# Performance work log

Hardware: AMD Instinct MI355X
Metric: run time of the kernel (lower is better)

Reference implementation:

```python
import jax, jax.numpy as jnp
import numpy as np

SELF_OBS_DIM = 18
NBR_OBS_DIM = 6
K = 6          # num_use_neighbor_obs
H = 128        # neighbor_hidden_size
B = 65536


def _mlp2(x, w1, b1, w2, b2):
    # two fc layers each followed by tanh nonlinearity
    x = jnp.tanh(x @ w1 + b1)
    return jnp.tanh(x @ w2 + b2)


def setup_inputs() -> dict:
    key = jax.random.key(0)
    ks = jax.random.split(key, 12)

    def w(k, i, o):
        return jax.random.normal(k, (i, o), dtype=jnp.float32) * (1.0 / np.sqrt(i))

    return {
        "self_obs": jax.random.normal(ks[0], (B, SELF_OBS_DIM), dtype=jnp.float32),
        "obs": jax.random.normal(ks[1], (B, SELF_OBS_DIM + K * NBR_OBS_DIM), dtype=jnp.float32),
        # embedding_mlp: (self_obs_dim + nbr_obs_dim) -> H -> H
        "e_w1": w(ks[2], SELF_OBS_DIM + NBR_OBS_DIM, H), "e_b1": jnp.zeros((H,), jnp.float32),
        "e_w2": w(ks[3], H, H), "e_b2": jnp.zeros((H,), jnp.float32),
        # neighbor_value_mlp: H -> H -> H
        "v_w1": w(ks[4], H, H), "v_b1": jnp.zeros((H,), jnp.float32),
        "v_w2": w(ks[5], H, H), "v_b2": jnp.zeros((H,), jnp.float32),
        # attention_mlp: 2H -> H -> H -> 1
        "a_w1": w(ks[6], 2 * H, H), "a_b1": jnp.zeros((H,), jnp.float32),
        "a_w2": w(ks[7], H, H), "a_b2": jnp.zeros((H,), jnp.float32),
        "a_w3": w(ks[8], H, 1), "a_b3": jnp.zeros((1,), jnp.float32),
        "all_neighbor_obs_size": K * NBR_OBS_DIM,
        "batch_size": B,
    }


def reference(self_obs, obs, e_w1, e_b1, e_w2, e_b2, v_w1, v_b1, v_w2, v_b2,
              a_w1, a_b1, a_w2, a_b2, a_w3, a_b3, all_neighbor_obs_size, batch_size):
    # slice neighbor obs and flatten: row i -> (batch i//K, neighbor i%K)
    obs_neighbors = obs[:, SELF_OBS_DIM:SELF_OBS_DIM + all_neighbor_obs_size]
    obs_neighbors = obs_neighbors.reshape(-1, NBR_OBS_DIM)            # [B*K, 6]
    # torch .repeat(K, 1): tile whole batch K times -> row i -> batch i % B
    self_obs_repeat = jnp.tile(self_obs, (K, 1))                       # [B*K, 18]
    mlp_input = jnp.concatenate((self_obs_repeat, obs_neighbors), axis=1)

    neighbor_embeddings = _mlp2(mlp_input, e_w1, e_b1, e_w2, e_b2)     # [B*K, H]
    neighbor_values = _mlp2(neighbor_embeddings, v_w1, v_b1, v_w2, v_b2)

    emb_mean = jnp.mean(neighbor_embeddings.reshape(batch_size, -1, H), axis=1)  # [B, H]
    emb_mean_repeat = jnp.tile(emb_mean, (K, 1))                       # [B*K, H]

    att_in = jnp.concatenate((neighbor_embeddings, emb_mean_repeat), axis=1)     # [B*K, 2H]
    att_h = jnp.tanh(att_in @ a_w1 + a_b1)
    att_h = jnp.tanh(att_h @ a_w2 + a_b2)
    att_logits = (att_h @ a_w3 + a_b3).reshape(batch_size, -1)         # [B, K]

    att = jax.nn.softmax(att_logits, axis=1).reshape(-1, 1)            # [B*K, 1]
    weighted = (att * neighbor_values).reshape(batch_size, -1, H)      # [B, K, H]
    return jnp.sum(weighted, axis=1)                                   # [B, H]
```

## Files before the change

### kernel.cpp

```cpp
#include <hip/hip_runtime.h>

typedef _Float16 f16;
typedef f16   f16x8 __attribute__((ext_vector_type(8)));
typedef float f32x4 __attribute__((ext_vector_type(4)));
typedef unsigned int uint;

#define NB     65536
#define TPB    16

#define OFF_E1 0
#define OFF_E2 4096
#define OFF_V1 20480
#define OFF_V2 36864
#define OFF_A1 53248
#define OFF_A2 86016
#define WFRAG_TOTAL 102400

#define EMB_BYTE_OFF   204800ull
#define PERM_BYTE_OFF  (204800ull + 100663296ull)

#define LDS_FENCE() asm volatile("s_waitcnt lgkmcnt(0)" ::: "memory")
#define WAIT_VM0()  asm volatile("s_waitcnt vmcnt(0)" ::: "memory")
#define BAR()       { __builtin_amdgcn_s_barrier(); __builtin_amdgcn_sched_barrier(0); }
#define SBAR()      __builtin_amdgcn_sched_barrier(0)

__device__ __forceinline__ float tanh_fast(float x) {
  float e = __expf(2.0f * x);
  return 1.0f - 2.0f * __builtin_amdgcn_rcpf(e + 1.0f);
}

__global__ void prep_weights(const float* __restrict__ e1, const float* __restrict__ e2,
                             const float* __restrict__ v1, const float* __restrict__ v2,
                             const float* __restrict__ a1, const float* __restrict__ a2,
                             f16* __restrict__ dst)
{
  int i = blockIdx.x * 256 + threadIdx.x;
  if (i >= WFRAG_TOTAL) return;
  const float* src; int base, Ksrc;
  if      (i < OFF_E2) { src = e1; base = OFF_E1; Ksrc = 24;  }
  else if (i < OFF_V1) { src = e2; base = OFF_E2; Ksrc = 128; }
  else if (i < OFF_V2) { src = v1; base = OFF_V1; Ksrc = 128; }
  else if (i < OFF_A1) { src = v2; base = OFF_V2; Ksrc = 128; }
  else if (i < OFF_A2) { src = a1; base = OFF_A1; Ksrc = 256; }
  else                 { src = a2; base = OFF_A2; Ksrc = 128; }
  int li   = i - base;
  int j    = li & 7;
  int lane = (li >> 3) & 63;
  int nt   = (li >> 9) & 7;
  int kc   = li >> 12;
  int k = kc*32 + (lane >> 4)*8 + j;
  int n = nt*16 + (lane & 15);
  float v = (k < Ksrc) ? src[k*128 + n] : 0.0f;
  dst[i] = (f16)v;
}

__device__ __forceinline__ void mfma2(f32x4* acc, f16x8 a0, f16x8 a1, const f16* Wb, int lane)
{
  #pragma unroll
  for (int nt = 0; nt < 8; ++nt) {
    f16x8 w = *(const f16x8*)(Wb + (nt*64 + lane)*8);
    acc[nt] = __builtin_amdgcn_mfma_f32_16x16x32_f16(a0, w, acc[nt], 0, 0, 0);
  }
  #pragma unroll
  for (int nt = 0; nt < 8; ++nt) {
    f16x8 w = *(const f16x8*)(Wb + ((8+nt)*64 + lane)*8);
    acc[nt] = __builtin_amdgcn_mfma_f32_16x16x32_f16(a1, w, acc[nt], 0, 0, 0);
  }
}

__device__ __forceinline__ void epi_tanh_store(char* tb, const f32x4* acc, const float* bias8,
                                               int wid, int lane)
{
  int col0 = lane & 15, q = lane >> 4;
  #pragma unroll
  for (int nt = 0; nt < 8; ++nt) {
    #pragma unroll
    for (int rg = 0; rg < 4; ++rg) {
      int row = wid*16 + q*4 + rg;
      float h = tanh_fast(acc[nt][rg] + bias8[nt]);
      int byte = (row*256 + (nt*16 + col0)*2) ^ ((row & 7) << 4);
      *(f16*)(tb + byte) = (f16)h;
    }
  }
}

__device__ __forceinline__ void read_h_frags(const char* tb, f16x8* frag, int wid, int lane)
{
  int c = lane >> 4, rr = lane & 15;
  int row = wid*16 + rr;
  #pragma unroll
  for (int kc = 0; kc < 4; ++kc) {
    int byte = (row*256 + kc*64 + c*16) ^ ((row & 7) << 4);
    frag[kc] = *(const f16x8*)(tb + byte);
  }
}

__device__ __forceinline__ void gload_lds16(const f16* g, f16* l) {
  __builtin_amdgcn_global_load_lds(
    (const __attribute__((address_space(1))) unsigned int*)g,
    (__attribute__((address_space(3))) unsigned int*)l, 16, 0, 0);
}
__device__ __forceinline__ void stage32(const f16* g, f16* l, int tid) {
  #pragma unroll
  for (int it = 0; it < 6; ++it) {
    int idx = (tid + it*384) & 2047;
    gload_lds16(g + idx*8, l + idx*8);
  }
}
__device__ __forceinline__ void stageE1(const f16* g, f16* l, int tid) {
  #pragma unroll
  for (int it = 0; it < 2; ++it) {
    int idx = (tid + it*384) & 511;
    gload_lds16(g + idx*8, l + idx*8);
  }
}

__device__ __forceinline__ f16x8 gather_x(const float* __restrict__ so, const float* __restrict__ obs,
                                          int r, int c)
{
  int rs = r & (NB - 1);
  uint rq = (uint)r / 6u;
  uint rm = (uint)r - rq*6u;
  float xv[8] = {0.f,0.f,0.f,0.f,0.f,0.f,0.f,0.f};
  if (c == 0) {
    #pragma unroll
    for (int j = 0; j < 8; ++j) xv[j] = so[rs*18 + j];
  } else if (c == 1) {
    #pragma unroll
    for (int j = 0; j < 8; ++j) xv[j] = so[rs*18 + 8 + j];
  } else if (c == 2) {
    xv[0] = so[rs*18 + 16];
    xv[1] = so[rs*18 + 17];
    const float* nb = obs + (size_t)rq*54 + 18 + rm*6;
    #pragma unroll
    for (int j = 0; j < 6; ++j) xv[2+j] = nb[j];
  }
  f16x8 f;
  #pragma unroll
  for (int j = 0; j < 8; ++j) f[j] = (f16)xv[j];
  return f;
}

__global__ void __launch_bounds__(384, 1) enc_kernel(
  const float* __restrict__ self_obs, const float* __restrict__ obs,
  const float* __restrict__ e_b1, const float* __restrict__ e_b2,
  const float* __restrict__ a_b1,
  const f16* __restrict__ wfrag, f16* __restrict__ emb_out, f16* __restrict__ perm_out)
{
  __shared__ __align__(16) f16 E1b[4096];
  __shared__ __align__(16) f16 E2b[16384];
  __shared__ __align__(16) f16 A1m[16384];
  __shared__ __align__(16) char tbuf[24576];
  __shared__ __align__(16) char mbuf[24576];

  int tid = threadIdx.x, lane = tid & 63, wid = tid >> 6;
  int c = lane >> 4, rr = lane & 15;

  stageE1(wfrag + OFF_E1, E1b, tid);
  stage32(wfrag + OFF_E2, E2b, tid);
  stage32(wfrag + OFF_A1 + 16384, A1m, tid);

  float eb1r[8], eb2r[8], ab1r[8];
  #pragma unroll
  for (int nt = 0; nt < 8; ++nt) {
    int col = nt*16 + rr;
    eb1r[nt] = e_b1[col]; eb2r[nt] = e_b2[col]; ab1r[nt] = a_b1[col];
  }

  int S = blockIdx.x;
  int T0 = S*6;
  int jmax = 4096 - T0; if (jmax > 6) jmax = 6;

  f16x8 xfrag = gather_x(self_obs, obs, T0*96 + wid*16 + rr, c);
  WAIT_VM0(); BAR();

  for (int j = 0; j < jmax; ++j) {
    int T = T0 + j;
    f32x4 acc1[8];
    #pragma unroll
    for (int nt = 0; nt < 8; ++nt) acc1[nt] = (f32x4){0.f,0.f,0.f,0.f};
    #pragma unroll
    for (int nt = 0; nt < 8; ++nt) {
      f16x8 w = *(const f16x8*)(E1b + (nt*64 + lane)*8);
      acc1[nt] = __builtin_amdgcn_mfma_f32_16x16x32_f16(xfrag, w, acc1[nt], 0, 0, 0);
    }
    epi_tanh_store(tbuf, acc1, eb1r, wid, lane);
    LDS_FENCE();
    f16x8 hf[4];
    read_h_frags(tbuf, hf, wid, lane);

    f16x8 xnext = xfrag;
    if (j + 1 < jmax) xnext = gather_x(self_obs, obs, (T+1)*96 + wid*16 + rr, c);

    f32x4 acc2[8];
    #pragma unroll
    for (int nt = 0; nt < 8; ++nt) acc2[nt] = (f32x4){0.f,0.f,0.f,0.f};
    mfma2(acc2, hf[0], hf[1], E2b,        lane);
    mfma2(acc2, hf[2], hf[3], E2b + 8192, lane);
    epi_tanh_store(tbuf, acc2, eb2r, wid, lane);
    LDS_FENCE();

    {
      size_t gbase = (size_t)T * (96*128);
      #pragma unroll
      for (int it = 0; it < 4; ++it) {
        int idx = it*64 + lane;
        int row = wid*16 + (idx >> 4), ch = idx & 15;
        int byte = (row*256 + ch*16) ^ ((row & 7) << 4);
        *(uint4*)(emb_out + gbase + (size_t)row*128 + ch*8) = *(const uint4*)(tbuf + byte);
      }
    }
    BAR();
    for (int i2 = tid; i2 < 1024; i2 += 384) {
      int b = i2 >> 6, cp = i2 & 63;
      float s0 = 0.f, s1 = 0.f;
      #pragma unroll
      for (int k2 = 0; k2 < 6; ++k2) {
        int brow = b*6 + k2;
        uint v = *(const uint*)(tbuf + ((brow*256 + cp*4) ^ ((brow & 7) << 4)));
        s0 += (float)__builtin_bit_cast(f16, (unsigned short)(v & 0xffff));
        s1 += (float)__builtin_bit_cast(f16, (unsigned short)(v >> 16));
      }
      f16 h0 = (f16)(s0 * (1.0f/6.0f)), h1 = (f16)(s1 * (1.0f/6.0f));
      uint mv = (uint)__builtin_bit_cast(unsigned short, h0)
              | ((uint)__builtin_bit_cast(unsigned short, h1) << 16);
      int mrow = j*16 + b;
      *(uint*)(mbuf + ((mrow*256 + cp*4) ^ ((mrow & 7) << 4))) = mv;
    }
    LDS_FENCE(); BAR();
    xfrag = xnext;
  }

  f16x8 mfr[4];
  read_h_frags(mbuf, mfr, wid, lane);
  f32x4 accm[8];
  #pragma unroll
  for (int nt = 0; nt < 8; ++nt) accm[nt] = (f32x4){0.f,0.f,0.f,0.f};
  mfma2(accm, mfr[0], mfr[1], A1m,        lane);
  mfma2(accm, mfr[2], mfr[3], A1m + 8192, lane);

  int gbase = S*96;
  #pragma unroll
  for (int rg = 0; rg < 4; ++rg) {
    int m = gbase + wid*16 + c*4 + rg;
    if (m < NB) {
      f16x8 v;
      #pragma unroll
      for (int nt = 0; nt < 8; ++nt) v[nt] = (f16)(accm[nt][rg] + ab1r[nt]);
      *(f16x8*)(perm_out + (size_t)m*128 + rr*8) = v;
    }
  }
}

__global__ void __launch_bounds__(384, 1) att_kernel(
  const f16* __restrict__ wfrag, const f16* __restrict__ emb, const f16* __restrict__ perm,
  const float* __restrict__ a_b2, const float* __restrict__ a_w3, const float* __restrict__ a_b3,
  const float* __restrict__ v_b1, const float* __restrict__ v_b2,
  float* __restrict__ out)
{
  __shared__ __align__(16) f16 W[4][16384];
  __shared__ __align__(16) char tbuf[24576];
  __shared__ float attv[96];

  int tid = threadIdx.x, lane = tid & 63, wid = tid >> 6;
  int c = lane >> 4, rr = lane & 15;

  stage32(wfrag + OFF_A1, &W[0][0], tid);
  stage32(wfrag + OFF_A2, &W[1][0], tid);
  stage32(wfrag + OFF_V1, &W[2][0], tid);
  stage32(wfrag + OFF_V2, &W[3][0], tid);

  float ab2r[8], aw3r[8], vb1r[8], vb2r[8];
  #pragma unroll
  for (int nt = 0; nt < 8; ++nt) {
    int col = nt*16 + rr;
    ab2r[nt] = a_b2[col]; aw3r[nt] = a_w3[col]; vb1r[nt] = v_b1[col]; vb2r[nt] = v_b2[col];
  }
  float ab3r = a_b3[0];

  int t0 = blockIdx.x * TPB;
  f16x8 ef[4], mh[4];
  {
    size_t r = (size_t)t0*96 + wid*16 + rr;
    #pragma unroll
    for (int kc = 0; kc < 4; ++kc) ef[kc] = *(const f16x8*)(emb + r*128 + kc*32 + c*8);
    #pragma unroll
    for (int rg = 0; rg < 4; ++rg) {
      int m = (t0*96 + wid*16 + c*4 + rg) & (NB - 1);
      mh[rg] = *(const f16x8*)(perm + (size_t)m*128 + rr*8);
    }
  }
  WAIT_VM0(); BAR();

  for (int i = 0; i < TPB; ++i) {
    int t = t0 + i;

    f32x4 acc3[8];
    #pragma unroll
    for (int nt = 0; nt < 8; ++nt) acc3[nt] = (f32x4){0.f,0.f,0.f,0.f};
    mfma2(acc3, ef[0], ef[1], &W[0][0],    lane);
    mfma2(acc3, ef[2], ef[3], &W[0][8192], lane);

    f16x8 efn[4], mhn[4];
    {
      int tn = (i+1 < TPB) ? (t+1) : t;
      size_t r = (size_t)tn*96 + wid*16 + rr;
      #pragma unroll
      for (int kc = 0; kc < 4; ++kc) efn[kc] = *(const f16x8*)(emb + r*128 + kc*32 + c*8);
      #pragma unroll
      for (int rg = 0; rg < 4; ++rg) {
        int m = (tn*96 + wid*16 + c*4 + rg) & (NB - 1);
        mhn[rg] = *(const f16x8*)(perm + (size_t)m*128 + rr*8);
      }
    }

    #pragma unroll
    for (int nt = 0; nt < 8; ++nt) {
      #pragma unroll
      for (int rg = 0; rg < 4; ++rg) {
        int row = wid*16 + c*4 + rg;
        float h = tanh_fast(acc3[nt][rg] + (float)mh[rg][nt]);
        int byte = (row*256 + (nt*16 + rr)*2) ^ ((row & 7) << 4);
        *(f16*)(tbuf + byte) = (f16)h;
      }
    }
    LDS_FENCE();
    f16x8 hf[4];
    read_h_frags(tbuf, hf, wid, lane);

    f32x4 acc4[8];
    #pragma unroll
    for (int nt = 0; nt < 8; ++nt) acc4[nt] = (f32x4){0.f,0.f,0.f,0.f};
    mfma2(acc4, hf[0], hf[1], &W[1][0],    lane);
    mfma2(acc4, hf[2], hf[3], &W[1][8192], lane);

    float part[4] = {0.f,0.f,0.f,0.f};
    #pragma unroll
    for (int nt = 0; nt < 8; ++nt) {
      #pragma unroll
      for (int rg = 0; rg < 4; ++rg) part[rg] += tanh_fast(acc4[nt][rg] + ab2r[nt]) * aw3r[nt];
    }
    #pragma unroll
    for (int rg = 0; rg < 4; ++rg) {
      part[rg] += __shfl_xor(part[rg], 1);
      part[rg] += __shfl_xor(part[rg], 2);
      part[rg] += __shfl_xor(part[rg], 4);
      part[rg] += __shfl_xor(part[rg], 8);
    }
    if (rr == 0) {
      #pragma unroll
      for (int rg = 0; rg < 4; ++rg) attv[wid*16 + c*4 + rg] = part[rg] + ab3r;
    }
    LDS_FENCE(); BAR();
    if (tid < 16) {
      float l[6]; float m = -1e30f;
      #pragma unroll
      for (int k2 = 0; k2 < 6; ++k2) { l[k2] = attv[tid*6 + k2]; m = fmaxf(m, l[k2]); }
      float ss = 0.f;
      #pragma unroll
      for (int k2 = 0; k2 < 6; ++k2) { l[k2] = __expf(l[k2] - m); ss += l[k2]; }
      float inv = __builtin_amdgcn_rcpf(ss);
      #pragma unroll
      for (int k2 = 0; k2 < 6; ++k2) attv[tid*6 + k2] = l[k2] * inv;
    }
    LDS_FENCE(); BAR();
    float attw[4];
    #pragma unroll
    for (int rg = 0; rg < 4; ++rg) attw[rg] = attv[wid*16 + c*4 + rg];

    f32x4 acc5[8];
    #pragma unroll
    for (int nt = 0; nt < 8; ++nt) acc5[nt] = (f32x4){0.f,0.f,0.f,0.f};
    mfma2(acc5, ef[0], ef[1], &W[2][0],    lane);
    mfma2(acc5, ef[2], ef[3], &W[2][8192], lane);
    epi_tanh_store(tbuf, acc5, vb1r, wid, lane);
    LDS_FENCE();
    read_h_frags(tbuf, hf, wid, lane);

    f32x4 acc6[8];
    #pragma unroll
    for (int nt = 0; nt < 8; ++nt) acc6[nt] = (f32x4){0.f,0.f,0.f,0.f};
    mfma2(acc6, hf[0], hf[1], &W[3][0],    lane);
    mfma2(acc6, hf[2], hf[3], &W[3][8192], lane);

    #pragma unroll
    for (int nt = 0; nt < 8; ++nt) {
      #pragma unroll
      for (int rg = 0; rg < 4; ++rg) {
        int brow = wid*16 + c*4 + rg;
        float v = tanh_fast(acc6[nt][rg] + vb2r[nt]) * attw[rg];
        int byte = (brow*256 + (nt*16 + rr)*2) ^ ((brow & 7) << 4);
        *(f16*)(tbuf + byte) = (f16)v;
      }
    }
    LDS_FENCE(); BAR();

    int b0 = t*16;
    for (int i2 = tid; i2 < 1024; i2 += 384) {
      int b = i2 >> 6, cp = i2 & 63;
      float s0 = 0.f, s1 = 0.f;
      #pragma unroll
      for (int k2 = 0; k2 < 6; ++k2) {
        int brow = b*6 + k2;
        uint v = *(const uint*)(tbuf + ((brow*256 + cp*4) ^ ((brow & 7) << 4)));
        s0 += (float)__builtin_bit_cast(f16, (unsigned short)(v & 0xffff));
        s1 += (float)__builtin_bit_cast(f16, (unsigned short)(v >> 16));
      }
      float2 st = {s0, s1};
      *(float2*)(out + (size_t)(b0 + b)*128 + cp*2) = st;
    }
    BAR();

    #pragma unroll
    for (int kc = 0; kc < 4; ++kc) ef[kc] = efn[kc];
    #pragma unroll
    for (int rg = 0; rg < 4; ++rg) mh[rg] = mhn[rg];
  }
}

extern "C" void kernel_launch(void* const* d_in, const int* in_sizes, int n_in,
                              void* d_out, int out_size, void* d_ws, size_t ws_size,
                              hipStream_t stream)
{
  const float* self_obs = (const float*)d_in[0];
  const float* obs  = (const float*)d_in[1];
  const float* e_w1 = (const float*)d_in[2];
  const float* e_b1 = (const float*)d_in[3];
  const float* e_w2 = (const float*)d_in[4];
  const float* e_b2 = (const float*)d_in[5];
  const float* v_w1 = (const float*)d_in[6];
  const float* v_b1 = (const float*)d_in[7];
  const float* v_w2 = (const float*)d_in[8];
  const float* v_b2 = (const float*)d_in[9];
  const float* a_w1 = (const float*)d_in[10];
  const float* a_b1 = (const float*)d_in[11];
  const float* a_w2 = (const float*)d_in[12];
  const float* a_b2 = (const float*)d_in[13];
  const float* a_w3 = (const float*)d_in[14];
  const float* a_b3 = (const float*)d_in[15];

  f16*   wfrag = (f16*)d_ws;
  f16*   emb   = (f16*)((char*)d_ws + EMB_BYTE_OFF);
  f16*   perm  = (f16*)((char*)d_ws + PERM_BYTE_OFF);
  float* out   = (float*)d_out;

  prep_weights<<<400, 256, 0, stream>>>(e_w1, e_w2, v_w1, v_w2, a_w1, a_w2, wfrag);
  enc_kernel<<<683, 384, 0, stream>>>(self_obs, obs, e_b1, e_b2, a_b1, wfrag, emb, perm);
  att_kernel<<<256, 384, 0, stream>>>(wfrag, emb, perm, a_b2, a_w3, a_b3, v_b1, v_b2, out);
}
```

Baseline: 332.1 us.

## Make attention kernel wave-independent with per-wave jobs and in-register softmax

Restructures the attention kernel so each wave owns a 48-row job (8 batch items) with its own LDS scratch buffer. Softmax runs in registers through shuffles, and output sums are accumulated per wave, which removes the block-wide barriers and the shared attv buffer. It moves to 7 waves per block and drops the a_b3 bias, since softmax is shift invariant. It also drops the next-tile register prefetch of emb/perm, so global load latency is exposed inside each job, and raises register pressure with three chunks of fragments held live.

```diff
diff --git a/kernel.cpp b/kernel.cpp
--- a/kernel.cpp
+++ b/kernel.cpp
@@ -22,7 +22,6 @@
 #define LDS_FENCE() asm volatile("s_waitcnt lgkmcnt(0)" ::: "memory")
 #define WAIT_VM0()  asm volatile("s_waitcnt vmcnt(0)" ::: "memory")
 #define BAR()       { __builtin_amdgcn_s_barrier(); __builtin_amdgcn_sched_barrier(0); }
-#define SBAR()      __builtin_amdgcn_sched_barrier(0)
 
 __device__ __forceinline__ float tanh_fast(float x) {
   float e = __expf(2.0f * x);
@@ -252,23 +251,34 @@
   }
 }
 
-__global__ void __launch_bounds__(384, 1) att_kernel(
+#define NWAVE  7
+#define AITERS 5
+#define NJOBS  8192
+
+__global__ void __launch_bounds__(448, 1) att_kernel(
   const f16* __restrict__ wfrag, const f16* __restrict__ emb, const f16* __restrict__ perm,
-  const float* __restrict__ a_b2, const float* __restrict__ a_w3, const float* __restrict__ a_b3,
+  const float* __restrict__ a_b2, const float* __restrict__ a_w3,
   const float* __restrict__ v_b1, const float* __restrict__ v_b2,
   float* __restrict__ out)
 {
   __shared__ __align__(16) f16 W[4][16384];
-  __shared__ __align__(16) char tbuf[24576];
-  __shared__ float attv[96];
+  __shared__ __align__(16) char tbuf[NWAVE][4096];
 
   int tid = threadIdx.x, lane = tid & 63, wid = tid >> 6;
   int c = lane >> 4, rr = lane & 15;
 
-  stage32(wfrag + OFF_A1, &W[0][0], tid);
-  stage32(wfrag + OFF_A2, &W[1][0], tid);
-  stage32(wfrag + OFF_V1, &W[2][0], tid);
-  stage32(wfrag + OFF_V2, &W[3][0], tid);
+  {
+    const int offs[4] = {OFF_A1, OFF_A2, OFF_V1, OFF_V2};
+    #pragma unroll
+    for (int m = 0; m < 4; ++m) {
+      const f16* s = wfrag + offs[m];
+      #pragma unroll
+      for (int it = 0; it < 5; ++it) {
+        int idx = (tid + it*448) & 2047;
+        gload_lds16(s + idx*8, &W[m][0] + idx*8);
+      }
+    }
+  }
 
   float ab2r[8], aw3r[8], vb1r[8], vb2r[8];
   #pragma unroll
@@ -276,145 +286,163 @@
     int col = nt*16 + rr;
     ab2r[nt] = a_b2[col]; aw3r[nt] = a_w3[col]; vb1r[nt] = v_b1[col]; vb2r[nt] = v_b2[col];
   }
-  float ab3r = a_b3[0];
-
-  int t0 = blockIdx.x * TPB;
-  f16x8 ef[4], mh[4];
-  {
-    size_t r = (size_t)t0*96 + wid*16 + rr;
-    #pragma unroll
-    for (int kc = 0; kc < 4; ++kc) ef[kc] = *(const f16x8*)(emb + r*128 + kc*32 + c*8);
-    #pragma unroll
-    for (int rg = 0; rg < 4; ++rg) {
-      int m = (t0*96 + wid*16 + c*4 + rg) & (NB - 1);
-      mh[rg] = *(const f16x8*)(perm + (size_t)m*128 + rr*8);
-    }
-  }
+
   WAIT_VM0(); BAR();
 
-  for (int i = 0; i < TPB; ++i) {
-    int t = t0 + i;
-
-    f32x4 acc3[8];
-    #pragma unroll
-    for (int nt = 0; nt < 8; ++nt) acc3[nt] = (f32x4){0.f,0.f,0.f,0.f};
-    mfma2(acc3, ef[0], ef[1], &W[0][0],    lane);
-    mfma2(acc3, ef[2], ef[3], &W[0][8192], lane);
-
-    f16x8 efn[4], mhn[4];
-    {
-      int tn = (i+1 < TPB) ? (t+1) : t;
-      size_t r = (size_t)tn*96 + wid*16 + rr;
-      #pragma unroll
-      for (int kc = 0; kc < 4; ++kc) efn[kc] = *(const f16x8*)(emb + r*128 + kc*32 + c*8);
+  char* tb = (char*)&tbuf[wid][0];
+
+  for (int it = 0; it < AITERS; ++it) {
+    int job = (blockIdx.x * AITERS + it) * NWAVE + wid;
+    if (job >= NJOBS) break;
+    int rbase = job * 48;
+
+    f16x8 ef[3][4];
+    float E[3][4];
+    #pragma unroll
+    for (int ch = 0; ch < 3; ++ch) {
+      int ra = rbase + ch*16 + rr;
+      #pragma unroll
+      for (int kc = 0; kc < 4; ++kc)
+        ef[ch][kc] = *(const f16x8*)(emb + (size_t)ra*128 + kc*32 + c*8);
+      f16x8 mh[4];
       #pragma unroll
       for (int rg = 0; rg < 4; ++rg) {
-        int m = (tn*96 + wid*16 + c*4 + rg) & (NB - 1);
-        mhn[rg] = *(const f16x8*)(perm + (size_t)m*128 + rr*8);
-      }
-    }
-
-    #pragma unroll
-    for (int nt = 0; nt < 8; ++nt) {
+        int m = (rbase + ch*16 + c*4 + rg) & (NB - 1);
+        mh[rg] = *(const f16x8*)(perm + (size_t)m*128 + rr*8);
+      }
+      f32x4 acc[8];
+      #pragma unroll
+      for (int nt = 0; nt < 8; ++nt) acc[nt] = (f32x4){0.f,0.f,0.f,0.f};
+      mfma2(acc, ef[ch][0], ef[ch][1], &W[0][0],    lane);
+      mfma2(acc, ef[ch][2], ef[ch][3], &W[0][8192], lane);
+      #pragma unroll
+      for (int nt = 0; nt < 8; ++nt) {
+        #pragma unroll
+        for (int rg = 0; rg < 4; ++rg) {
+          int row = c*4 + rg;
+          float h = tanh_fast(acc[nt][rg] + (float)mh[rg][nt]);
+          *(f16*)(tb + ((row*256 + (nt*16 + rr)*2) ^ ((row & 7) << 4))) = (f16)h;
+        }
+      }
+      LDS_FENCE();
+      f16x8 hf[4];
+      #pragma unroll
+      for (int kc = 0; kc < 4; ++kc)
+        hf[kc] = *(const f16x8*)(tb + ((rr*256 + kc*64 + c*16) ^ ((rr & 7) << 4)));
+      f32x4 acc2[8];
+      #pragma unroll
+      for (int nt = 0; nt < 8; ++nt) acc2[nt] = (f32x4){0.f,0.f,0.f,0.f};
+      mfma2(acc2, hf[0], hf[1], &W[1][0],    lane);
+      mfma2(acc2, hf[2], hf[3], &W[1][8192], lane);
+      float part[4] = {0.f,0.f,0.f,0.f};
+      #pragma unroll
+      for (int nt = 0; nt < 8; ++nt) {
+        #pragma unroll
+        for (int rg = 0; rg < 4; ++rg)
+          part[rg] += tanh_fast(acc2[nt][rg] + ab2r[nt]) * aw3r[nt];
+      }
       #pragma unroll
       for (int rg = 0; rg < 4; ++rg) {
-        int row = wid*16 + c*4 + rg;
-        float h = tanh_fast(acc3[nt][rg] + (float)mh[rg][nt]);
-        int byte = (row*256 + (nt*16 + rr)*2) ^ ((row & 7) << 4);
-        *(f16*)(tbuf + byte) = (f16)h;
-      }
-    }
-    LDS_FENCE();
-    f16x8 hf[4];
-    read_h_frags(tbuf, hf, wid, lane);
-
-    f32x4 acc4[8];
-    #pragma unroll
-    for (int nt = 0; nt < 8; ++nt) acc4[nt] = (f32x4){0.f,0.f,0.f,0.f};
-    mfma2(acc4, hf[0], hf[1], &W[1][0],    lane);
-    mfma2(acc4, hf[2], hf[3], &W[1][8192], lane);
-
-    float part[4] = {0.f,0.f,0.f,0.f};
-    #pragma unroll
-    for (int nt = 0; nt < 8; ++nt) {
-      #pragma unroll
-      for (int rg = 0; rg < 4; ++rg) part[rg] += tanh_fast(acc4[nt][rg] + ab2r[nt]) * aw3r[nt];
-    }
-    #pragma unroll
-    for (int rg = 0; rg < 4; ++rg) {
-      part[rg] += __shfl_xor(part[rg], 1);
-      part[rg] += __shfl_xor(part[rg], 2);
-      part[rg] += __shfl_xor(part[rg], 4);
-      part[rg] += __shfl_xor(part[rg], 8);
-    }
-    if (rr == 0) {
-      #pragma unroll
-      for (int rg = 0; rg < 4; ++rg) attv[wid*16 + c*4 + rg] = part[rg] + ab3r;
-    }
-    LDS_FENCE(); BAR();
-    if (tid < 16) {
-      float l[6]; float m = -1e30f;
-      #pragma unroll
-      for (int k2 = 0; k2 < 6; ++k2) { l[k2] = attv[tid*6 + k2]; m = fmaxf(m, l[k2]); }
-      float ss = 0.f;
-      #pragma unroll
-      for (int k2 = 0; k2 < 6; ++k2) { l[k2] = __expf(l[k2] - m); ss += l[k2]; }
-      float inv = __builtin_amdgcn_rcpf(ss);
-      #pragma unroll
-      for (int k2 = 0; k2 < 6; ++k2) attv[tid*6 + k2] = l[k2] * inv;
-    }
-    LDS_FENCE(); BAR();
-    float attw[4];
-    #pragma unroll
-    for (int rg = 0; rg < 4; ++rg) attw[rg] = attv[wid*16 + c*4 + rg];
-
-    f32x4 acc5[8];
-    #pragma unroll
-    for (int nt = 0; nt < 8; ++nt) acc5[nt] = (f32x4){0.f,0.f,0.f,0.f};
-    mfma2(acc5, ef[0], ef[1], &W[2][0],    lane);
-    mfma2(acc5, ef[2], ef[3], &W[2][8192], lane);
-    epi_tanh_store(tbuf, acc5, vb1r, wid, lane);
-    LDS_FENCE();
-    read_h_frags(tbuf, hf, wid, lane);
-
-    f32x4 acc6[8];
-    #pragma unroll
-    for (int nt = 0; nt < 8; ++nt) acc6[nt] = (f32x4){0.f,0.f,0.f,0.f};
-    mfma2(acc6, hf[0], hf[1], &W[3][0],    lane);
-    mfma2(acc6, hf[2], hf[3], &W[3][8192], lane);
-
-    #pragma unroll
-    for (int nt = 0; nt < 8; ++nt) {
+        part[rg] += __shfl_xor(part[rg], 1);
+        part[rg] += __shfl_xor(part[rg], 2);
+        part[rg] += __shfl_xor(part[rg], 4);
+        part[rg] += __shfl_xor(part[rg], 8);
+        E[ch][rg] = __expf(part[rg]);
+      }
+    }
+
+    int g = rr & 7;
+    float pg = 0.f;
+    #pragma unroll
+    for (int ch = 0; ch < 3; ++ch) {
       #pragma unroll
       for (int rg = 0; rg < 4; ++rg) {
-        int brow = wid*16 + c*4 + rg;
-        float v = tanh_fast(acc6[nt][rg] + vb2r[nt]) * attw[rg];
-        int byte = (brow*256 + (nt*16 + rr)*2) ^ ((brow & 7) << 4);
-        *(f16*)(tbuf + byte) = (f16)v;
-      }
-    }
-    LDS_FENCE(); BAR();
-
-    int b0 = t*16;
-    for (int i2 = tid; i2 < 1024; i2 += 384) {
-      int b = i2 >> 6, cp = i2 & 63;
-      float s0 = 0.f, s1 = 0.f;
-      #pragma unroll
-      for (int k2 = 0; k2 < 6; ++k2) {
-        int brow = b*6 + k2;
-        uint v = *(const uint*)(tbuf + ((brow*256 + cp*4) ^ ((brow & 7) << 4)));
-        s0 += (float)__builtin_bit_cast(f16, (unsigned short)(v & 0xffff));
-        s1 += (float)__builtin_bit_cast(f16, (unsigned short)(v >> 16));
-      }
-      float2 st = {s0, s1};
-      *(float2*)(out + (size_t)(b0 + b)*128 + cp*2) = st;
-    }
-    BAR();
-
-    #pragma unroll
-    for (int kc = 0; kc < 4; ++kc) ef[kc] = efn[kc];
-    #pragma unroll
-    for (int rg = 0; rg < 4; ++rg) mh[rg] = mhn[rg];
+        int r = ch*16 + c*4 + rg;
+        pg += (r/6 == g) ? E[ch][rg] : 0.f;
+      }
+    }
+    pg += __shfl_xor(pg, 16);
+    pg += __shfl_xor(pg, 32);
+    float invS = __builtin_amdgcn_rcpf(pg);
+    float attw[3][4];
+    #pragma unroll
+    for (int ch = 0; ch < 3; ++ch) {
+      #pragma unroll
+      for (int rg = 0; rg < 4; ++rg) {
+        int r = ch*16 + c*4 + rg;
+        attw[ch][rg] = E[ch][rg] * __shfl(invS, r/6);
+      }
+    }
+
+    float o0x=0.f,o0y=0.f,o1x=0.f,o1y=0.f,o2x=0.f,o2y=0.f,o3x=0.f,o3y=0.f;
+    float o4x=0.f,o4y=0.f,o5x=0.f,o5y=0.f,o6x=0.f,o6y=0.f,o7x=0.f,o7y=0.f;
+    #pragma unroll
+    for (int ch = 0; ch < 3; ++ch) {
+      f32x4 acc3[8];
+      #pragma unroll
+      for (int nt = 0; nt < 8; ++nt) acc3[nt] = (f32x4){0.f,0.f,0.f,0.f};
+      mfma2(acc3, ef[ch][0], ef[ch][1], &W[2][0],    lane);
+      mfma2(acc3, ef[ch][2], ef[ch][3], &W[2][8192], lane);
+      #pragma unroll
+      for (int nt = 0; nt < 8; ++nt) {
+        #pragma unroll
+        for (int rg = 0; rg < 4; ++rg) {
+          int row = c*4 + rg;
+          float h = tanh_fast(acc3[nt][rg] + vb1r[nt]);
+          *(f16*)(tb + ((row*256 + (nt*16 + rr)*2) ^ ((row & 7) << 4))) = (f16)h;
+        }
+      }
+      LDS_FENCE();
+      f16x8 hf[4];
+      #pragma unroll
+      for (int kc = 0; kc < 4; ++kc)
+        hf[kc] = *(const f16x8*)(tb + ((rr*256 + kc*64 + c*16) ^ ((rr & 7) << 4)));
+      f32x4 acc4[8];
+      #pragma unroll
+      for (int nt = 0; nt < 8; ++nt) acc4[nt] = (f32x4){0.f,0.f,0.f,0.f};
+      mfma2(acc4, hf[0], hf[1], &W[3][0],    lane);
+      mfma2(acc4, hf[2], hf[3], &W[3][8192], lane);
+      #pragma unroll
+      for (int nt = 0; nt < 8; ++nt) {
+        #pragma unroll
+        for (int rg = 0; rg < 4; ++rg) {
+          int row = c*4 + rg;
+          float v = tanh_fast(acc4[nt][rg] + vb2r[nt]) * attw[ch][rg];
+          *(f16*)(tb + ((row*256 + (nt*16 + rr)*2) ^ ((row & 7) << 4))) = (f16)v;
+        }
+      }
+      LDS_FENCE();
+      #pragma unroll
+      for (int rl = 0; rl < 16; ++rl) {
+        uint v = *(const uint*)(tb + ((rl*256 + lane*4) ^ ((rl & 7) << 4)));
+        float lo = (float)__builtin_bit_cast(f16, (unsigned short)(v & 0xffff));
+        float hi = (float)__builtin_bit_cast(f16, (unsigned short)(v >> 16));
+        constexpr int gmap0[16] = {0,0,0,0,0,0,1,1,1,1,1,1,2,2,2,2};
+        constexpr int gmap1[16] = {2,2,3,3,3,3,3,3,4,4,4,4,4,4,5,5};
+        constexpr int gmap2[16] = {5,5,5,5,6,6,6,6,6,6,7,7,7,7,7,7};
+        int gg = (ch == 0) ? gmap0[rl] : (ch == 1) ? gmap1[rl] : gmap2[rl];
+        switch (gg) {
+          case 0: o0x += lo; o0y += hi; break;
+          case 1: o1x += lo; o1y += hi; break;
+          case 2: o2x += lo; o2y += hi; break;
+          case 3: o3x += lo; o3y += hi; break;
+          case 4: o4x += lo; o4y += hi; break;
+          case 5: o5x += lo; o5y += hi; break;
+          case 6: o6x += lo; o6y += hi; break;
+          default: o7x += lo; o7y += hi; break;
+        }
+      }
+      LDS_FENCE();
+    }
+    size_t ob = (size_t)(job*8)*128 + lane*2;
+    { float2 s = {o0x,o0y}; *(float2*)(out + ob + 0*128) = s; }
+    { float2 s = {o1x,o1y}; *(float2*)(out + ob + 1*128) = s; }
+    { float2 s = {o2x,o2y}; *(float2*)(out + ob + 2*128) = s; }
+    { float2 s = {o3x,o3y}; *(float2*)(out + ob + 3*128) = s; }
+    { float2 s = {o4x,o4y}; *(float2*)(out + ob + 4*128) = s; }
+    { float2 s = {o5x,o5y}; *(float2*)(out + ob + 5*128) = s; }
+    { float2 s = {o6x,o6y}; *(float2*)(out + ob + 6*128) = s; }
+    { float2 s = {o7x,o7y}; *(float2*)(out + ob + 7*128) = s; }
   }
 }
 
@@ -437,7 +465,6 @@
   const float* a_w2 = (const float*)d_in[12];
   const float* a_b2 = (const float*)d_in[13];
   const float* a_w3 = (const float*)d_in[14];
-  const float* a_b3 = (const float*)d_in[15];
 
   f16*   wfrag = (f16*)d_ws;
   f16*   emb   = (f16*)((char*)d_ws + EMB_BYTE_OFF);
@@ -446,5 +473,5 @@
 
   prep_weights<<<400, 256, 0, stream>>>(e_w1, e_w2, v_w1, v_w2, a_w1, a_w2, wfrag);
   enc_kernel<<<683, 384, 0, stream>>>(self_obs, obs, e_b1, e_b2, a_b1, wfrag, emb, perm);
-  att_kernel<<<256, 384, 0, stream>>>(wfrag, emb, perm, a_b2, a_w3, a_b3, v_b1, v_b2, out);
-}
+  att_kernel<<<256, 448, 0, stream>>>(wfrag, emb, perm, a_b2, a_w3, v_b1, v_b2, out);
+}
```

New measurement: 304.7 us. -8.3%, faster.
